# Kernel optimization log

Measured on AMD Instinct MI355X. Metric: run time of the kernel, lower is better.

## Reference

```python
import jax, jax.numpy as jnp
import numpy as np

NUM_HEADS = 16

def setup_inputs() -> dict:
    key = jax.random.key(0)
    ks = jax.random.split(key, 10)
    B, S, D = 2, 2048, 1024
    q = jax.random.normal(ks[0], (B, S, D), dtype=jnp.float32)
    k = jax.random.normal(ks[1], (B, S, D), dtype=jnp.float32)
    v = jax.random.normal(ks[2], (B, S, D), dtype=jnp.float32)
    mask = jax.random.randint(ks[3], (B, S), 0, 2, dtype=jnp.int32)
    scale = 0.02
    Wq = jax.random.normal(ks[4], (D, D), dtype=jnp.float32) * scale
    bq = jax.random.normal(ks[5], (D,), dtype=jnp.float32) * scale
    Wk = jax.random.normal(ks[6], (D, D), dtype=jnp.float32) * scale
    bk = jax.random.normal(ks[7], (D,), dtype=jnp.float32) * scale
    Wv = jax.random.normal(ks[8], (D, D), dtype=jnp.float32) * scale
    bv = jax.random.normal(ks[9], (D,), dtype=jnp.float32) * scale
    return {"q": q, "k": k, "v": v, "mask": mask,
            "Wq": Wq, "bq": bq, "Wk": Wk, "bk": bk, "Wv": Wv, "bv": bv}


def reference(q, k, v, mask, Wq, bq, Wk, bk, Wv, bv):
    B, S, D = q.shape
    H = NUM_HEADS
    dh = D // H
    # per-head split along last dim == reshape to (B, S, H, dh)
    Qh = (q @ Wq + bq).reshape(B, S, H, dh)
    Kh = (k @ Wk + bk).reshape(B, S, H, dh)
    Vh = (v @ Wv + bv).reshape(B, S, H, dh)
    # NOTE: original scales by sqrt(10), not sqrt(dim_per_head)
    scores = jnp.einsum('bqhd,bkhd->bhqk', Qh, Kh) / jnp.sqrt(jnp.float32(10.0))
    # mask [B,S] masks key positions; masked_fill replaces with -1e9
    scores = jnp.where(mask[:, None, None, :] == 0, jnp.float32(-1e9), scores)
    probs = jax.nn.softmax(scores, axis=-1)
    out = jnp.einsum('bhqk,bkhd->bqhd', probs, Vh).reshape(B, S, D)
    return out
```

## Files before the change

kernel.cpp:

```cpp
#include <hip/hip_runtime.h>
#include <hip/hip_bf16.h>

typedef __attribute__((ext_vector_type(8))) short short8;
typedef __attribute__((ext_vector_type(4))) float f32x4;

#define SC_L2E 0.4561727848849353f

#if __has_builtin(__builtin_amdgcn_exp2f)
#define EXP2F __builtin_amdgcn_exp2f
#else
#define EXP2F exp2f
#endif

static __device__ __forceinline__ void gload16(const void* g, void* l) {
  __builtin_amdgcn_global_load_lds((const __attribute__((address_space(1))) void*)g,
                                   (__attribute__((address_space(3))) void*)l, 16, 0, 0);
}

__global__ void k_cvt(const float* __restrict__ q, const float* __restrict__ kk,
                      const float* __restrict__ v, __hip_bfloat16* __restrict__ xb,
                      const float* __restrict__ Wq, const float* __restrict__ Wk,
                      const float* __restrict__ Wv, __hip_bfloat16* __restrict__ wt,
                      const int* __restrict__ mask, float* __restrict__ bias2) {
  __shared__ float T[64][65];
  if (blockIdx.x < 6144) {
    const size_t i = ((size_t)blockIdx.x * 256 + threadIdx.x) * 8;
    const int t = (int)(i >> 22);
    const float* src = (t == 0) ? q : (t == 1) ? kk : v;
    const size_t off = i & 4194303u;
    float4 f0 = *(const float4*)(src + off);
    float4 f1 = *(const float4*)(src + off + 4);
    union { short8 s; __hip_bfloat16 h[8]; } u;
    u.h[0] = __float2bfloat16(f0.x); u.h[1] = __float2bfloat16(f0.y);
    u.h[2] = __float2bfloat16(f0.z); u.h[3] = __float2bfloat16(f0.w);
    u.h[4] = __float2bfloat16(f1.x); u.h[5] = __float2bfloat16(f1.y);
    u.h[6] = __float2bfloat16(f1.z); u.h[7] = __float2bfloat16(f1.w);
    *(short8*)((char*)xb + i * 2) = u.s;
    return;
  }
  const int idx2 = blockIdx.x - 6144;
  const int z = idx2 >> 8;
  const int r2 = idx2 & 255;
  const int bxi = r2 & 15, byi = r2 >> 4;
  if (z == 0 && byi == 0) {
    const int idx = bxi * 256 + threadIdx.x;
    bias2[idx] = mask[idx] ? -12.0f : -1e30f;
  }
  const float* W = (z == 0) ? Wq : (z == 1) ? Wk : Wv;
  __hip_bfloat16* Wd = wt + (size_t)z * 1048576;
  const int n0 = bxi * 64, k0 = byi * 64;
  const int tx = threadIdx.x & 63, ty = threadIdx.x >> 6;
#pragma unroll
  for (int r = 0; r < 16; ++r)
    T[ty + r * 4][tx] = W[(size_t)(k0 + ty + r * 4) * 1024 + n0 + tx];
  __syncthreads();
#pragma unroll
  for (int r = 0; r < 16; ++r)
    Wd[(size_t)(n0 + ty + r * 4) * 1024 + k0 + tx] = __float2bfloat16(T[tx][ty + r * 4]);
}

__global__ __launch_bounds__(256) void k_proj(
    const __hip_bfloat16* __restrict__ xb, const __hip_bfloat16* __restrict__ wt,
    const float* __restrict__ bq, const float* __restrict__ bk, const float* __restrict__ bv,
    __hip_bfloat16* __restrict__ Qb, __hip_bfloat16* __restrict__ Kb,
    __hip_bfloat16* __restrict__ Vt) {
  __shared__ char smem[32768];
  char* As = smem;
  char* Bs = smem + 16384;
  const int orig = blockIdx.x;
  const int xcd = orig & 7, idx = orig >> 3;
  const int by = xcd * 4 + (idx & 3);
  const int bx = (idx >> 2) & 7;
  const int t = idx >> 5;
  const char* X = (const char*)(xb + (size_t)t * 4194304);
  const char* W = (const char*)(wt + (size_t)t * 1048576);
  const float* bias = (t == 0) ? bq : (t == 1) ? bk : bv;
  const int m0 = by * 128, n0 = bx * 128;
  const int tid = threadIdx.x, w = tid >> 6, lane = tid & 63;
  const int l15 = lane & 15, g = lane >> 4;
  const int l8 = lane >> 3, l7 = lane & 7;
  const int vswz = ((l7 ^ l8) << 4);
  const int wm = (w >> 1) * 64, wn = (w & 1) * 64;
  f32x4 acc[4][4];
#pragma unroll
  for (int i = 0; i < 4; ++i)
#pragma unroll
    for (int j = 0; j < 4; ++j) acc[i][j] = (f32x4){0.f, 0.f, 0.f, 0.f};

  for (int k0 = 0; k0 < 2048; k0 += 128) {
    __syncthreads();
#pragma unroll
    for (int j = 0; j < 4; ++j) {
      const int ch = w * 4 + j;
      gload16(X + (size_t)(m0 + ch * 8 + l8) * 2048 + k0 + vswz, As + ch * 1024);
      gload16(W + (size_t)(n0 + ch * 8 + l8) * 2048 + k0 + vswz, Bs + ch * 1024);
    }
    __syncthreads();
#pragma unroll
    for (int kk = 0; kk < 2; ++kk) {
      short8 af[4], bf_[4];
#pragma unroll
      for (int mt = 0; mt < 4; ++mt) {
        const int row = wm + mt * 16 + l15;
        af[mt] = *(const short8*)(As + row * 128 + ((kk * 64 + g * 16) ^ ((row & 7) << 4)));
      }
#pragma unroll
      for (int nt = 0; nt < 4; ++nt) {
        const int row = wn + nt * 16 + l15;
        bf_[nt] = *(const short8*)(Bs + row * 128 + ((kk * 64 + g * 16) ^ ((row & 7) << 4)));
      }
#pragma unroll
      for (int mt = 0; mt < 4; ++mt)
#pragma unroll
        for (int nt = 0; nt < 4; ++nt)
          acc[mt][nt] = __builtin_amdgcn_mfma_f32_16x16x32_bf16(af[mt], bf_[nt], acc[mt][nt], 0, 0, 0);
    }
  }

  float bv4[4];
#pragma unroll
  for (int nt = 0; nt < 4; ++nt) bv4[nt] = bias[n0 + wn + nt * 16 + l15];

  if (t < 2) {
#pragma unroll
    for (int mt = 0; mt < 4; ++mt) {
#pragma unroll
      for (int nt = 0; nt < 4; ++nt) {
        const int feat = n0 + wn + nt * 16 + l15;
        const int h = feat >> 6, d = feat & 63;
#pragma unroll
        for (int r = 0; r < 4; ++r) {
          const int token = m0 + wm + mt * 16 + g * 4 + r;
          const int b = token >> 11, s = token & 2047;
          const float val = acc[mt][nt][r] + bv4[nt];
          const __hip_bfloat16 hb = __float2bfloat16(val);
          if (t == 0) Qb[((size_t)(b * 16 + h) * 2048 + s) * 64 + d] = hb;
          else        Kb[((size_t)(b * 16 + h) * 2048 + s) * 64 + d] = hb;
        }
      }
    }
  } else {
    __hip_bfloat16* T2 = (__hip_bfloat16*)smem;
    const int bb = m0 >> 11;
    const int s0 = m0 & 2047;
#pragma unroll
    for (int p = 0; p < 2; ++p) {
      __syncthreads();
      if ((w >> 1) == p) {
#pragma unroll
        for (int mt = 0; mt < 4; ++mt)
#pragma unroll
          for (int nt = 0; nt < 4; ++nt) {
            const int feat = wn + nt * 16 + l15;
#pragma unroll
            for (int r = 0; r < 4; ++r) {
              const int tok = mt * 16 + g * 4 + r;
              T2[feat * 64 + (tok ^ ((feat & 7) << 3))] =
                  __float2bfloat16(acc[mt][nt][r] + bv4[nt]);
            }
          }
      }
      __syncthreads();
#pragma unroll
      for (int sw = 0; sw < 4; ++sw) {
        const int row = sw * 32 + (tid >> 3);
        const int c = tid & 7;
        const short8 vchunk = *(const short8*)(smem + row * 128 + 16 * (c ^ (row & 7)));
        const int gfeat = n0 + row;
        const int hh = gfeat >> 6, dd = gfeat & 63;
        *(short8*)(Vt + ((size_t)((bb * 16 + hh) * 64 + dd)) * 2048 + s0 + p * 64 + c * 8) = vchunk;
      }
    }
  }
}

#define ATTN_BODY(CUR, PRF, DOPREF, SYNC)                                      \
  {                                                                            \
    float4 mb[4];                                                              \
    _Pragma("unroll") for (int nt = 0; nt < 4; ++nt)                           \
        mb[nt] = *(const float4*)(mbp + (nt >> 1) * 32 + ((nt & 1) << 2) + g * 8); \
    mbp += 64;                                                                 \
    __builtin_amdgcn_sched_barrier(0);       \
    if (DOPREF) {                                                              \
      _Pragma("unroll") for (int j = 0; j < 2; ++j) {                          \
        gload16(kst[j], Ks[PRF] + (w * 2 + j) * 1024);                         \
        gload16(vst[j], Vs[PRF] + (w * 2 + j) * 1024);                         \
      }                                                                        \
    }                                                                          \
    kst[0] += 8192; kst[1] += 8192; vst[0] += 128; vst[1] += 128;              \
    f32x4 sA[4], sB[4];                                                        \
    __builtin_amdgcn_s_setprio(1);                                             \
    _Pragma("unroll") for (int nt = 0; nt < 4; ++nt) {                         \
      const int key = nt * 16 + l15;                                           \
      const int ksw = (key & 7) << 4;                                          \
      const short8 kf0 = *(const short8*)(Ks[CUR] + key * 128 + ((g * 16) ^ ksw)); \
      const short8 kf1 = *(const short8*)(Ks[CUR] + key * 128 + ((64 + g * 16) ^ ksw)); \
      f32x4 z = (f32x4){0.f, 0.f, 0.f, 0.f};                                   \
      sA[nt] = __builtin_amdgcn_mfma_f32_16x16x32_bf16(kf0, aq[0][0], z, 0, 0, 0); \
      sA[nt] = __builtin_amdgcn_mfma_f32_16x16x32_bf16(kf1, aq[0][1], sA[nt], 0, 0, 0); \
      sB[nt] = __builtin_amdgcn_mfma_f32_16x16x32_bf16(kf0, aq[1][0], z, 0, 0, 0); \
      sB[nt] = __builtin_amdgcn_mfma_f32_16x16x32_bf16(kf1, aq[1][1], sB[nt], 0, 0, 0); \
    }                                                                          \
    __builtin_amdgcn_s_setprio(0);                                             \
    short8 pbA[2], pbB[2];                                                     \
    _Pragma("unroll") for (int c = 0; c < 2; ++c) {                            \
      union { short8 s8; __hip_bfloat16 hh[8]; } pa, pb;                       \
      _Pragma("unroll") for (int e = 0; e < 8; ++e) {                          \
        const int nt = 2 * c + (e >> 2);                                       \
        const float mbe = (e & 3) == 0 ? mb[nt].x : (e & 3) == 1 ? mb[nt].y :  \
                          (e & 3) == 2 ? mb[nt].z : mb[nt].w;                  \
        pa.hh[e] = __float2bfloat16(EXP2F(fmaf(sA[nt][e & 3], SC_L2E, mbe)));  \
        pb.hh[e] = __float2bfloat16(EXP2F(fmaf(sB[nt][e & 3], SC_L2E, mbe)));  \
      }                                                                        \
      pbA[c] = pa.s8; pbB[c] = pb.s8;                                          \
    }                                                                          \
    __builtin_amdgcn_s_setprio(1);                                             \
    laccA = __builtin_amdgcn_mfma_f32_16x16x32_bf16(ones8, pbA[0], laccA, 0, 0, 0); \
    laccA = __builtin_amdgcn_mfma_f32_16x16x32_bf16(ones8, pbA[1], laccA, 0, 0, 0); \
    laccB = __builtin_amdgcn_mfma_f32_16x16x32_bf16(ones8, pbB[0], laccB, 0, 0, 0); \
    laccB = __builtin_amdgcn_mfma_f32_16x16x32_bf16(ones8, pbB[1], laccB, 0, 0, 0); \
    _Pragma("unroll") for (int dt = 0; dt < 4; ++dt) {                         \
      const int d = dt * 16 + l15;                                             \
      const int sw2 = (d & 7) << 4;                                            \
      const short8 v0 = *(const short8*)(Vs[CUR] + d * 128 + ((g * 16) ^ sw2)); \
      const short8 v1 = *(const short8*)(Vs[CUR] + d * 128 + ((64 + g * 16) ^ sw2)); \
      f32x4 oa = oaccA[dt], ob = oaccB[dt];                                    \
      oa = __builtin_amdgcn_mfma_f32_16x16x32_bf16(v0, pbA[0], oa, 0, 0, 0);   \
      oa = __builtin_amdgcn_mfma_f32_16x16x32_bf16(v1, pbA[1], oa, 0, 0, 0);   \
      ob = __builtin_amdgcn_mfma_f32_16x16x32_bf16(v0, pbB[0], ob, 0, 0, 0);   \
      ob = __builtin_amdgcn_mfma_f32_16x16x32_bf16(v1, pbB[1], ob, 0, 0, 0);   \
      oaccA[dt] = oa; oaccB[dt] = ob;                                          \
    }                                                                          \
    __builtin_amdgcn_s_setprio(0);                                             \
    if (SYNC == 4) { asm volatile("s_waitcnt vmcnt(4)" ::: "memory"); }        \
    else if (SYNC == 0) { asm volatile("s_waitcnt vmcnt(0)" ::: "memory"); }   \
    if (SYNC >= 0) {                                                           \
      __builtin_amdgcn_s_barrier();                                            \
      __builtin_amdgcn_sched_barrier(0);                                       \
    }                                                                          \
  }

__global__ __launch_bounds__(256, 2) void k_attn(
    const __hip_bfloat16* __restrict__ Qb, const __hip_bfloat16* __restrict__ Kb,
    const __hip_bfloat16* __restrict__ Vt, const float* __restrict__ bias2,
    float* __restrict__ out) {
  __shared__ char Ks[3][8192];
  __shared__ char Vs[3][8192];
  const int orig = blockIdx.x;
  const int swz = (orig & 7) * 64 + (orig >> 3);
  const int bh = swz >> 4, qb = swz & 15;
  const int b = bh >> 4, h = bh & 15;
  const int tid = threadIdx.x, w = tid >> 6, lane = tid & 63;
  const int g = lane >> 4, l15 = lane & 15;
  const char* Qc = (const char*)(Qb + (size_t)bh * 131072);
  const char* Kc = (const char*)(Kb + (size_t)bh * 131072);
  const char* Vc = (const char*)(Vt + (size_t)bh * 131072);

  const int l8 = lane >> 3, l7 = lane & 7;
  const int vswz = ((l7 ^ l8) << 4);

  short8 aq[2][2];
  const int arow0 = qb * 128 + w * 32 + l15;
#pragma unroll
  for (int qt = 0; qt < 2; ++qt)
#pragma unroll
    for (int kc = 0; kc < 2; ++kc)
      aq[qt][kc] = *(const short8*)(Qc + (size_t)(arow0 + qt * 16) * 128 + kc * 64 + g * 16);

  f32x4 oaccA[4], oaccB[4];
#pragma unroll
  for (int i = 0; i < 4; ++i) {
    oaccA[i] = (f32x4){0.f, 0.f, 0.f, 0.f};
    oaccB[i] = (f32x4){0.f, 0.f, 0.f, 0.f};
  }
  f32x4 laccA = (f32x4){0.f, 0.f, 0.f, 0.f};
  f32x4 laccB = (f32x4){0.f, 0.f, 0.f, 0.f};
  const short8 ones8 = {(short)0x3F80, (short)0x3F80, (short)0x3F80, (short)0x3F80,
                        (short)0x3F80, (short)0x3F80, (short)0x3F80, (short)0x3F80};

  const char* kst[2];
  const char* vst[2];
#pragma unroll
  for (int j = 0; j < 2; ++j) {
    const int ch = w * 2 + j;
    const int s = ch * 8 + l8;
    const int nt0 = s >> 4, gg = (s >> 2) & 3, rr = s & 3;
    const int kap = (nt0 >> 1) * 32 + gg * 8 + ((nt0 & 1) << 2) + rr;
    kst[j] = Kc + (size_t)kap * 128 + vswz;
    vst[j] = Vc + (size_t)s * 4096 + vswz;
  }
#pragma unroll
  for (int tpre = 0; tpre < 2; ++tpre) {
#pragma unroll
    for (int j = 0; j < 2; ++j) {
      gload16(kst[j], Ks[tpre] + (w * 2 + j) * 1024);
      gload16(vst[j], Vs[tpre] + (w * 2 + j) * 1024);
    }
    kst[0] += 8192; kst[1] += 8192; vst[0] += 128; vst[1] += 128;
  }
  asm volatile("s_waitcnt vmcnt(4)" ::: "memory");
  __builtin_amdgcn_s_barrier();
  __builtin_amdgcn_sched_barrier(0);

  const float* mbp = bias2 + b * 2048;
  for (int k = 0; k < 10; ++k) {
    ATTN_BODY(0, 2, 1, 4)
    ATTN_BODY(1, 0, 1, 4)
    ATTN_BODY(2, 1, 1, 4)
  }
  ATTN_BODY(0, 2, 0, 0)
  ATTN_BODY(1, 0, 0, -1)

  const float rlA = 1.0f / laccA[0];
  const float rlB = 1.0f / laccB[0];
  float* orowA = out + ((size_t)(b * 2048 + arow0)) * 1024 + h * 64;
  float* orowB = orowA + 16 * 1024;
#pragma unroll
  for (int dt = 0; dt < 4; ++dt) {
    float4 stA, stB;
    stA.x = oaccA[dt][0] * rlA; stA.y = oaccA[dt][1] * rlA;
    stA.z = oaccA[dt][2] * rlA; stA.w = oaccA[dt][3] * rlA;
    stB.x = oaccB[dt][0] * rlB; stB.y = oaccB[dt][1] * rlB;
    stB.z = oaccB[dt][2] * rlB; stB.w = oaccB[dt][3] * rlB;
    *(float4*)(orowA + dt * 16 + g * 4) = stA;
    *(float4*)(orowB + dt * 16 + g * 4) = stB;
  }
}

extern "C" void kernel_launch(void* const* d_in, const int* in_sizes, int n_in,
                              void* d_out, int out_size, void* d_ws, size_t ws_size,
                              hipStream_t stream) {
  const float* q   = (const float*)d_in[0];
  const float* k   = (const float*)d_in[1];
  const float* v   = (const float*)d_in[2];
  const int* mask  = (const int*)d_in[3];
  const float* Wq  = (const float*)d_in[4];
  const float* bq  = (const float*)d_in[5];
  const float* Wk  = (const float*)d_in[6];
  const float* bk  = (const float*)d_in[7];
  const float* Wv  = (const float*)d_in[8];
  const float* bv  = (const float*)d_in[9];
  float* out = (float*)d_out;
  char* ws = (char*)d_ws;
  __hip_bfloat16* Xb = (__hip_bfloat16*)(ws);
  __hip_bfloat16* Wt = (__hip_bfloat16*)(ws + 25165824);
  __hip_bfloat16* Qb = (__hip_bfloat16*)(ws + 31457280);
  __hip_bfloat16* Kb = (__hip_bfloat16*)(ws + 39845888);
  __hip_bfloat16* Vt = (__hip_bfloat16*)(ws + 48234496);
  float* bias2      = (float*)(ws + 56623104);

  k_cvt<<<dim3(6912), dim3(256), 0, stream>>>(q, k, v, Xb, Wq, Wk, Wv, Wt, mask, bias2);
  k_proj<<<dim3(768), dim3(256), 0, stream>>>(Xb, Wt, bq, bk, bv, Qb, Kb, Vt);
  k_attn<<<dim3(512), dim3(256), 0, stream>>>(Qb, Kb, Vt, bias2, out);
}
```

Measured before the change: 102.4 us.

## Load V tiles directly from global into registers instead of staging through LDS

V fragments for the PV MFMA are now read straight from global memory into per-thread registers one tile ahead, replacing the async global-to-LDS copy and the LDS reads. This removes the V shared-memory buffers (halving LDS use) and the LDS read traffic for V, and the vmcnt wait counts are retuned for the mixed K-async plus V register loads. In exchange V loads are uncoalesced 16-byte per-lane reads with more global latency exposed per iteration, and register pressure rises.

```diff
diff --git a/kernel.cpp b/kernel.cpp
--- a/kernel.cpp
+++ b/kernel.cpp
@@ -174,20 +174,18 @@
   }
 }
 
-#define ATTN_BODY(CUR, PRF, DOPREF, SYNC)                                      \
+#define ATTN_BODY(CUR, PRF, DOK, DOV, VM)                                      \
   {                                                                            \
     float4 mb[4];                                                              \
     _Pragma("unroll") for (int nt = 0; nt < 4; ++nt)                           \
         mb[nt] = *(const float4*)(mbp + (nt >> 1) * 32 + ((nt & 1) << 2) + g * 8); \
     mbp += 64;                                                                 \
     __builtin_amdgcn_sched_barrier(0);       \
-    if (DOPREF) {                                                              \
-      _Pragma("unroll") for (int j = 0; j < 2; ++j) {                          \
+    if (DOK) {                                                                 \
+      _Pragma("unroll") for (int j = 0; j < 2; ++j)                            \
         gload16(kst[j], Ks[PRF] + (w * 2 + j) * 1024);                         \
-        gload16(vst[j], Vs[PRF] + (w * 2 + j) * 1024);                         \
-      }                                                                        \
-    }                                                                          \
-    kst[0] += 8192; kst[1] += 8192; vst[0] += 128; vst[1] += 128;              \
+    }                                                                          \
+    kst[0] += 8192; kst[1] += 8192;                                            \
     f32x4 sA[4], sB[4];                                                        \
     __builtin_amdgcn_s_setprio(1);                                             \
     _Pragma("unroll") for (int nt = 0; nt < 4; ++nt) {                         \
@@ -220,21 +218,24 @@
     laccB = __builtin_amdgcn_mfma_f32_16x16x32_bf16(ones8, pbB[0], laccB, 0, 0, 0); \
     laccB = __builtin_amdgcn_mfma_f32_16x16x32_bf16(ones8, pbB[1], laccB, 0, 0, 0); \
     _Pragma("unroll") for (int dt = 0; dt < 4; ++dt) {                         \
-      const int d = dt * 16 + l15;                                             \
-      const int sw2 = (d & 7) << 4;                                            \
-      const short8 v0 = *(const short8*)(Vs[CUR] + d * 128 + ((g * 16) ^ sw2)); \
-      const short8 v1 = *(const short8*)(Vs[CUR] + d * 128 + ((64 + g * 16) ^ sw2)); \
       f32x4 oa = oaccA[dt], ob = oaccB[dt];                                    \
-      oa = __builtin_amdgcn_mfma_f32_16x16x32_bf16(v0, pbA[0], oa, 0, 0, 0);   \
-      oa = __builtin_amdgcn_mfma_f32_16x16x32_bf16(v1, pbA[1], oa, 0, 0, 0);   \
-      ob = __builtin_amdgcn_mfma_f32_16x16x32_bf16(v0, pbB[0], ob, 0, 0, 0);   \
-      ob = __builtin_amdgcn_mfma_f32_16x16x32_bf16(v1, pbB[1], ob, 0, 0, 0);   \
+      oa = __builtin_amdgcn_mfma_f32_16x16x32_bf16(vr0[dt], pbA[0], oa, 0, 0, 0); \
+      oa = __builtin_amdgcn_mfma_f32_16x16x32_bf16(vr1[dt], pbA[1], oa, 0, 0, 0); \
+      ob = __builtin_amdgcn_mfma_f32_16x16x32_bf16(vr0[dt], pbB[0], ob, 0, 0, 0); \
+      ob = __builtin_amdgcn_mfma_f32_16x16x32_bf16(vr1[dt], pbB[1], ob, 0, 0, 0); \
       oaccA[dt] = oa; oaccB[dt] = ob;                                          \
     }                                                                          \
     __builtin_amdgcn_s_setprio(0);                                             \
-    if (SYNC == 4) { asm volatile("s_waitcnt vmcnt(4)" ::: "memory"); }        \
-    else if (SYNC == 0) { asm volatile("s_waitcnt vmcnt(0)" ::: "memory"); }   \
-    if (SYNC >= 0) {                                                           \
+    if (DOV) {                                                                 \
+      _Pragma("unroll") for (int dt = 0; dt < 4; ++dt) {                       \
+        vr0[dt] = *(const short8*)(vp[dt]);                                    \
+        vr1[dt] = *(const short8*)(vp[dt] + 64);                               \
+        vp[dt] += 128;                                                         \
+      }                                                                        \
+    }                                                                          \
+    if (VM == 10) { asm volatile("s_waitcnt vmcnt(10)" ::: "memory"); }        \
+    else if (VM == 8) { asm volatile("s_waitcnt vmcnt(8)" ::: "memory"); }     \
+    if (VM >= 0) {                                                             \
       __builtin_amdgcn_s_barrier();                                            \
       __builtin_amdgcn_sched_barrier(0);                                       \
     }                                                                          \
@@ -245,7 +246,6 @@
     const __hip_bfloat16* __restrict__ Vt, const float* __restrict__ bias2,
     float* __restrict__ out) {
   __shared__ char Ks[3][8192];
-  __shared__ char Vs[3][8192];
   const int orig = blockIdx.x;
   const int swz = (orig & 7) * 64 + (orig >> 3);
   const int bh = swz >> 4, qb = swz & 15;
@@ -279,7 +279,6 @@
                         (short)0x3F80, (short)0x3F80, (short)0x3F80, (short)0x3F80};
 
   const char* kst[2];
-  const char* vst[2];
 #pragma unroll
   for (int j = 0; j < 2; ++j) {
     const int ch = w * 2 + j;
@@ -287,29 +286,38 @@
     const int nt0 = s >> 4, gg = (s >> 2) & 3, rr = s & 3;
     const int kap = (nt0 >> 1) * 32 + gg * 8 + ((nt0 & 1) << 2) + rr;
     kst[j] = Kc + (size_t)kap * 128 + vswz;
-    vst[j] = Vc + (size_t)s * 4096 + vswz;
-  }
+  }
+  const char* vp[4];
+#pragma unroll
+  for (int dt = 0; dt < 4; ++dt)
+    vp[dt] = Vc + (size_t)(dt * 16 + l15) * 4096 + g * 16;
+  short8 vr0[4], vr1[4];
+
 #pragma unroll
   for (int tpre = 0; tpre < 2; ++tpre) {
 #pragma unroll
-    for (int j = 0; j < 2; ++j) {
+    for (int j = 0; j < 2; ++j)
       gload16(kst[j], Ks[tpre] + (w * 2 + j) * 1024);
-      gload16(vst[j], Vs[tpre] + (w * 2 + j) * 1024);
-    }
-    kst[0] += 8192; kst[1] += 8192; vst[0] += 128; vst[1] += 128;
-  }
-  asm volatile("s_waitcnt vmcnt(4)" ::: "memory");
+    kst[0] += 8192; kst[1] += 8192;
+  }
+#pragma unroll
+  for (int dt = 0; dt < 4; ++dt) {
+    vr0[dt] = *(const short8*)(vp[dt]);
+    vr1[dt] = *(const short8*)(vp[dt] + 64);
+    vp[dt] += 128;
+  }
+  asm volatile("s_waitcnt vmcnt(10)" ::: "memory");
   __builtin_amdgcn_s_barrier();
   __builtin_amdgcn_sched_barrier(0);
 
   const float* mbp = bias2 + b * 2048;
   for (int k = 0; k < 10; ++k) {
-    ATTN_BODY(0, 2, 1, 4)
-    ATTN_BODY(1, 0, 1, 4)
-    ATTN_BODY(2, 1, 1, 4)
-  }
-  ATTN_BODY(0, 2, 0, 0)
-  ATTN_BODY(1, 0, 0, -1)
+    ATTN_BODY(0, 2, 1, 1, 10)
+    ATTN_BODY(1, 0, 1, 1, 10)
+    ATTN_BODY(2, 1, 1, 1, 10)
+  }
+  ATTN_BODY(0, 2, 0, 1, 8)
+  ATTN_BODY(1, 0, 0, 0, -1)
 
   const float rlA = 1.0f / laccA[0];
   const float rlB = 1.0f / laccB[0];
```

New measurement: 132.6 us. 1.29x slower.
